# Performance work log

Hardware: AMD Instinct MI355X
Metric: run time of the kernel (lower is better)

Reference implementation:

```python
import jax, jax.numpy as jnp
import numpy as np

DEPTH = 8
INPUT_WIDTH = 64
INNER_WIDTH = 32
BATCH = 65536
N_NODES = 2 ** DEPTH - 1   # 255 inner nodes
N_LEAVES = 2 ** DEPTH      # 256 bins
EPS = 1e-8


def _tree_paths(depth):
    """For each leaf, the inner-node index at each level and whether the path
    goes right (right child uses 1 - decision, mirroring hstack([p, 1-p]) indexing)."""
    node_idx = np.zeros((2 ** depth, depth), dtype=np.int32)
    is_right = np.zeros((2 ** depth, depth), dtype=bool)
    for leaf in range(2 ** depth):
        idx = 0
        for level in range(depth):
            bit = (leaf >> (depth - 1 - level)) & 1
            node_idx[leaf, level] = idx
            is_right[leaf, level] = bool(bit)
            idx = 2 * idx + 1 + bit
    return node_idx, is_right

_NODE_IDX_NP, _IS_RIGHT_NP = _tree_paths(DEPTH)
NODE_IDX = jnp.asarray(_NODE_IDX_NP)   # [L, depth]
IS_RIGHT = jnp.asarray(_IS_RIGHT_NP)   # [L, depth]


def _init_b_i():
    """Replicates PartialRadialLayer.init_tree_weights: thresholds evenly dividing [0,1],
    stored as logits so sigmoid(b_i) recovers the threshold."""
    b = np.zeros(N_NODES, dtype=np.float64)
    b[0] = -0.5
    used = 1
    for i in range(1, DEPTH):
        n_nodes = 2 ** i
        div = float(2 ** (i + 1))
        for node in range(n_nodes):
            b[used + node] = -(2 * node + 1) / div
        used += n_nodes
    return np.log(-b / (1.0 + b)).astype(np.float32).reshape(1, -1)


def setup_inputs() -> dict:
    key = jax.random.key(0)
    kx, kr, kt = jax.random.split(key, 3)
    x = jax.random.normal(kx, (BATCH, INPUT_WIDTH), dtype=jnp.float32)
    # kaiming_normal_ on [1, input_width]: fan_in = input_width
    ray = jax.random.normal(kr, (1, INPUT_WIDTH), dtype=jnp.float32) * np.sqrt(2.0 / INPUT_WIDTH)
    # kaiming_normal_ on [L, I, W]: fan_in = I * W
    inner_transforms = jax.random.normal(kt, (N_LEAVES, INPUT_WIDTH, INNER_WIDTH), dtype=jnp.float32) * np.sqrt(2.0 / (INPUT_WIDTH * INNER_WIDTH))
    w_i = jnp.zeros((1, N_NODES), dtype=jnp.float32)
    a_i = 5.0 * jnp.ones((1, N_NODES), dtype=jnp.float32)
    b_i = jnp.asarray(_init_b_i())
    return {"x": x, "ray": ray, "inner_transforms": inner_transforms,
            "w_i": w_i, "b_i": b_i, "a_i": a_i}


def reference(x, ray, inner_transforms, w_i, b_i, a_i):
    # angles: arccos(cosine_similarity(x, ray)) / pi
    x_norm = jnp.maximum(jnp.linalg.norm(x, axis=1), EPS)            # [B]
    r_norm = jnp.maximum(jnp.linalg.norm(ray, axis=1), EPS)          # [1]
    cos = jnp.clip((x @ ray[0]) / (x_norm * r_norm), -1.0, 1.0)      # [B]
    angles = jnp.arccos(cos) / jnp.pi                                # [B]

    # per-node decisions
    node_fns = (0.5 + jax.nn.sigmoid(w_i)) * angles[:, None] - jax.nn.sigmoid(b_i)  # [B, N]
    decisions = jax.nn.sigmoid(node_fns * (1.0 + a_i))                               # [B, N]

    # soft bin distribution: product along each root-to-leaf path
    g = decisions[:, NODE_IDX]                       # [B, L, depth]
    vals = jnp.where(IS_RIGHT, 1.0 - g, g)           # right child -> 1 - p
    distribution = jnp.prod(vals, axis=2)            # [B, L]

    # weighted per-leaf transforms: einsum('bi,liw->blw') then ('bl,blo->bo'), fused
    out = jnp.einsum('bl,bi,liw->bw', distribution, x, inner_transforms)
    return out
```

## Files before the change

kernel.cpp:

```cpp
#include <hip/hip_runtime.h>
#include <hip/hip_bf16.h>

#define NLEAF 256
#define MBLK 256
#define THREADS 512

typedef __attribute__((ext_vector_type(4))) float f32x4;
typedef __attribute__((ext_vector_type(4))) unsigned int uint4v;
typedef __attribute__((ext_vector_type(8))) __bf16 bf16x8;
typedef __attribute__((ext_vector_type(4))) __bf16 bf16x4;

#define OFF_DIST 0
#define OFF_XP   131072
#define OFF_T    147456
#define OFF_AC   151552
#define OFF_BC   152576
#define OFF_ANG  153600
#define OFF_RAY  154624
#define SMEM_BYTES 154880

__device__ __forceinline__ float sigf(float s) { return 1.0f / (1.0f + __expf(-s)); }

__global__ void prep_T(const float* __restrict__ T, __bf16* __restrict__ wsT) {
  int gid = blockIdx.x * 256 + threadIdx.x;
  int l = gid >> 11;
  int rem = gid & 2047;
  int k = rem >> 5;
  int w = rem & 31;
  float v = T[gid];
  int off = (w * 128 + 2 * k) ^ ((w & 7) << 4);
  wsT[((size_t)l * 4096 + off) >> 1] = (__bf16)v;
}

template <bool USE_WS>
__global__ __launch_bounds__(THREADS, 2)
void prl_main(const float* __restrict__ x, const float* __restrict__ ray,
              const float* __restrict__ w_i, const float* __restrict__ b_i,
              const float* __restrict__ a_i, const void* __restrict__ tsrc,
              float* __restrict__ out) {
  extern __shared__ char smem[];
  const int tid = threadIdx.x;
  const int lane = tid & 63;
  const int wid = tid >> 6;
  const int g = lane >> 4;
  const int ln = lane & 15;
  const int row0 = blockIdx.x * MBLK;

  float* A_c = (float*)(smem + OFF_AC);
  float* B_c = (float*)(smem + OFF_BC);
  float* angles = (float*)(smem + OFF_ANG);
  float* ray_l = (float*)(smem + OFF_RAY);
  __bf16* distb = (__bf16*)(smem + OFF_DIST);

  if (tid < 255) {
    float aa = 1.0f + a_i[tid];
    A_c[tid] = (0.5f + sigf(w_i[tid])) * aa;
    B_c[tid] = -sigf(b_i[tid]) * aa;
  }
  if (tid >= 256 && tid < 320) ray_l[tid - 256] = ray[tid - 256];
  __syncthreads();

  bf16x8 afrag[2][2] = {};
  float* xp = (float*)(smem + OFF_XP);
  for (int c = 0; c < 4; ++c) {
    const float* xg = x + (size_t)(row0 + c * 64) * 64;
#pragma unroll
    for (int p = 0; p < 2; ++p) {
      int idx = p * 512 + tid;
      f32x4 v = *(const f32x4*)(xg + idx * 4);
      *(f32x4*)(xp + idx * 4) = v;
      int cg = idx & 15;
      f32x4 rv = *(const f32x4*)(ray_l + cg * 4);
      float a0 = v[0] * v[0] + v[1] * v[1] + v[2] * v[2] + v[3] * v[3];
      float a1 = v[0] * rv[0] + v[1] * rv[1] + v[2] * rv[2] + v[3] * rv[3];
      float a2 = rv[0] * rv[0] + rv[1] * rv[1] + rv[2] * rv[2] + rv[3] * rv[3];
#pragma unroll
      for (int s = 1; s < 16; s <<= 1) {
        a0 += __shfl_xor(a0, s, 64);
        a1 += __shfl_xor(a1, s, 64);
        a2 += __shfl_xor(a2, s, 64);
      }
      if ((tid & 15) == 0) {
        int r = idx >> 4;
        float xn = fmaxf(sqrtf(a0), 1e-8f);
        float rn = fmaxf(sqrtf(a2), 1e-8f);
        float cs = a1 / (xn * rn);
        cs = fminf(fmaxf(cs, -1.0f), 1.0f);
        angles[c * 64 + r] = acosf(cs) * 0.31830988618379067f;
      }
    }
    __syncthreads();
    if ((wid >> 1) == c) {
#pragma unroll
      for (int mt = 0; mt < 2; ++mt)
#pragma unroll
        for (int kt = 0; kt < 2; ++kt) {
          int rl = (wid & 1) * 32 + mt * 16 + ln;
          int k0 = kt * 32 + g * 8;
          f32x4 u0 = *(const f32x4*)(xp + rl * 64 + k0);
          f32x4 u1 = *(const f32x4*)(xp + rl * 64 + k0 + 4);
          bf16x8 af;
          af[0] = (__bf16)u0[0]; af[1] = (__bf16)u0[1];
          af[2] = (__bf16)u0[2]; af[3] = (__bf16)u0[3];
          af[4] = (__bf16)u1[0]; af[5] = (__bf16)u1[1];
          af[6] = (__bf16)u1[2]; af[7] = (__bf16)u1[3];
          afrag[mt][kt] = af;
        }
    }
    __syncthreads();
  }

  __bf16* PA = (__bf16*)(smem + OFF_XP);
  __bf16* PB = (__bf16*)(smem + OFF_XP + 8192);
  if (tid < 256) {
    float ang = angles[tid];
    float d = sigf(fmaf(A_c[0], ang, B_c[0]));
    PA[tid] = (__bf16)d;
    PA[256 + tid] = (__bf16)(1.0f - d);
  }
  __syncthreads();
  {
    int n = tid >> 8, r = tid & 255;
    float p = (float)PA[tid];
    float ang = angles[r];
    float d = sigf(fmaf(A_c[1 + n], ang, B_c[1 + n]));
    PB[(2 * n) * 256 + r] = (__bf16)(p * d);
    PB[(2 * n + 1) * 256 + r] = (__bf16)(p * (1.0f - d));
  }
  __syncthreads();
#pragma unroll
  for (int it = 0; it < 2; ++it) {
    int e = it * 512 + tid;
    int n = e >> 8, r = e & 255;
    float p = (float)PB[e];
    float ang = angles[r];
    float d = sigf(fmaf(A_c[3 + n], ang, B_c[3 + n]));
    PA[(2 * n) * 256 + r] = (__bf16)(p * d);
    PA[(2 * n + 1) * 256 + r] = (__bf16)(p * (1.0f - d));
  }
  __syncthreads();
#pragma unroll
  for (int it = 0; it < 4; ++it) {
    int e = it * 512 + tid;
    int n = e >> 8, r = e & 255;
    float p = (float)PA[e];
    float ang = angles[r];
    float d = sigf(fmaf(A_c[7 + n], ang, B_c[7 + n]));
    PB[(2 * n) * 256 + r] = (__bf16)(p * d);
    PB[(2 * n + 1) * 256 + r] = (__bf16)(p * (1.0f - d));
  }
  __syncthreads();
#pragma unroll
  for (int it = 0; it < 8; ++it) {
    int e = it * 512 + tid;
    int n4 = e >> 8, r = e & 255;
    float p4 = (float)PB[e];
    float ang = angles[r];
    float d4 = sigf(fmaf(A_c[15 + n4], ang, B_c[15 + n4]));
    float p5[2] = {p4 * d4, p4 * (1.0f - d4)};
#pragma unroll
    for (int b5 = 0; b5 < 2; ++b5) {
      int n5 = 2 * n4 + b5;
      float d5 = sigf(fmaf(A_c[31 + n5], ang, B_c[31 + n5]));
      float p6[2] = {p5[b5] * d5, p5[b5] * (1.0f - d5)};
#pragma unroll
      for (int b6 = 0; b6 < 2; ++b6) {
        int n6 = 2 * n5 + b6;
        float d6 = sigf(fmaf(A_c[63 + n6], ang, B_c[63 + n6]));
        float p7[2] = {p6[b6] * d6, p6[b6] * (1.0f - d6)};
#pragma unroll
        for (int b7 = 0; b7 < 2; ++b7) {
          int n7 = 2 * n6 + b7;
          float d7 = sigf(fmaf(A_c[127 + n7], ang, B_c[127 + n7]));
          float pv = p7[b7];
          distb[(2 * n7) * 256 + r] = (__bf16)(pv * d7);
          distb[(2 * n7 + 1) * 256 + r] = (__bf16)(pv * (1.0f - d7));
        }
      }
    }
  }

  f32x4 acc[2][2] = {};
  const int strip = wid * 32;
  char* tb = smem + OFF_T;

  uint4v tv = {};
  f32x4 tvf = {};
  if constexpr (USE_WS) {
    if (tid < 256) tv = *(const uint4v*)((const char*)tsrc + tid * 16);
  } else {
    tvf = *(const f32x4*)((const float*)tsrc + tid * 4);
  }

  for (int l = 0; l < NLEAF; ++l) {
    __syncthreads();
    if constexpr (USE_WS) {
      if (tid < 256) *(uint4v*)(tb + tid * 16) = tv;
    } else {
      int e4 = tid * 4, k = e4 >> 5, wb = e4 & 31;
#pragma unroll
      for (int j = 0; j < 4; ++j) {
        int w = wb + j;
        int ad = (w * 128 + 2 * k) ^ ((w & 7) << 4);
        *(__bf16*)(tb + ad) = (__bf16)tvf[j];
      }
    }
    __syncthreads();
    if (l + 1 < NLEAF) {
      if constexpr (USE_WS) {
        if (tid < 256)
          tv = *(const uint4v*)((const char*)tsrc + (size_t)(l + 1) * 4096 + tid * 16);
      } else {
        tvf = *(const f32x4*)((const float*)tsrc + (size_t)(l + 1) * 2048 + tid * 4);
      }
    }
    bf16x8 bf[2][2];
#pragma unroll
    for (int kt = 0; kt < 2; ++kt)
#pragma unroll
      for (int nt = 0; nt < 2; ++nt) {
        int w = nt * 16 + ln;
        int ad = (w * 128 + kt * 64 + g * 16) ^ ((w & 7) << 4);
        bf[kt][nt] = *(const bf16x8*)(tb + ad);
      }
    f32x4 dv[2];
#pragma unroll
    for (int mt = 0; mt < 2; ++mt) {
      int row = strip + mt * 16 + g * 4;
      bf16x4 dd = *(const bf16x4*)(distb + l * 256 + row);
      dv[mt] = (f32x4){(float)dd[0], (float)dd[1], (float)dd[2], (float)dd[3]};
    }
    f32x4 zero = {0.0f, 0.0f, 0.0f, 0.0f};
#pragma unroll
    for (int mt = 0; mt < 2; ++mt)
#pragma unroll
      for (int nt = 0; nt < 2; ++nt) {
        f32x4 y = __builtin_amdgcn_mfma_f32_16x16x32_bf16(afrag[mt][0], bf[0][nt], zero, 0, 0, 0);
        y = __builtin_amdgcn_mfma_f32_16x16x32_bf16(afrag[mt][1], bf[1][nt], y, 0, 0, 0);
        acc[mt][nt] += dv[mt] * y;
      }
  }

#pragma unroll
  for (int mt = 0; mt < 2; ++mt)
#pragma unroll
    for (int nt = 0; nt < 2; ++nt)
#pragma unroll
      for (int e = 0; e < 4; ++e) {
        int row = row0 + strip + mt * 16 + g * 4 + e;
        out[(size_t)row * 32 + nt * 16 + ln] = acc[mt][nt][e];
      }
}

extern "C" void kernel_launch(void* const* d_in, const int* in_sizes, int n_in,
                              void* d_out, int out_size, void* d_ws, size_t ws_size,
                              hipStream_t stream) {
  const float* x = (const float*)d_in[0];
  const float* ray = (const float*)d_in[1];
  const float* T = (const float*)d_in[2];
  const float* w_i = (const float*)d_in[3];
  const float* b_i = (const float*)d_in[4];
  const float* a_i = (const float*)d_in[5];
  float* out = (float*)d_out;

  bool use_ws = ws_size >= (size_t)NLEAF * 4096;
  if (use_ws) {
    hipFuncSetAttribute(reinterpret_cast<const void*>(&prl_main<true>),
                        hipFuncAttributeMaxDynamicSharedMemorySize, SMEM_BYTES);
    prep_T<<<2048, 256, 0, stream>>>(T, (__bf16*)d_ws);
    prl_main<true><<<256, THREADS, SMEM_BYTES, stream>>>(x, ray, w_i, b_i, a_i, d_ws, out);
  } else {
    hipFuncSetAttribute(reinterpret_cast<const void*>(&prl_main<false>),
                        hipFuncAttributeMaxDynamicSharedMemorySize, SMEM_BYTES);
    prl_main<false><<<256, THREADS, SMEM_BYTES, stream>>>(x, ray, w_i, b_i, a_i, T, out);
  }
}
```

Baseline: 180.1 us.

## Double-buffer leaf transform tiles in LDS and coalesce prep_T writes

The main loop now keeps two LDS buffers for the per-leaf bf16 transform tile. The next leaf's tile is written while the current one feeds the MFMAs, so each iteration needs one barrier instead of two. prep_T is rewritten to use one block per leaf: it stages the swizzled tile in shared memory and writes it out as coalesced 16-byte stores instead of scattered 2-byte stores. The cost is 4 KB more LDS per block, which could affect occupancy at two blocks per CU.

Result: faster. 163.8 us (-9.1%).

```diff
diff --git a/kernel.cpp b/kernel.cpp
--- a/kernel.cpp
+++ b/kernel.cpp
@@ -13,23 +13,34 @@
 #define OFF_DIST 0
 #define OFF_XP   131072
 #define OFF_T    147456
-#define OFF_AC   151552
-#define OFF_BC   152576
-#define OFF_ANG  153600
-#define OFF_RAY  154624
-#define SMEM_BYTES 154880
+#define OFF_AC   155648
+#define OFF_BC   156672
+#define OFF_ANG  157696
+#define OFF_RAY  158720
+#define SMEM_BYTES 158976
 
 __device__ __forceinline__ float sigf(float s) { return 1.0f / (1.0f + __expf(-s)); }
 
-__global__ void prep_T(const float* __restrict__ T, __bf16* __restrict__ wsT) {
-  int gid = blockIdx.x * 256 + threadIdx.x;
-  int l = gid >> 11;
-  int rem = gid & 2047;
-  int k = rem >> 5;
-  int w = rem & 31;
-  float v = T[gid];
-  int off = (w * 128 + 2 * k) ^ ((w & 7) << 4);
-  wsT[((size_t)l * 4096 + off) >> 1] = (__bf16)v;
+__global__ __launch_bounds__(256) void prep_T(const float* __restrict__ T,
+                                              __bf16* __restrict__ wsT) {
+  __shared__ char tile[4096];
+  const int l = blockIdx.x;
+  const float* src = T + (size_t)l * 2048;
+  const int t = threadIdx.x;
+#pragma unroll
+  for (int p = 0; p < 2; ++p) {
+    int e = p * 1024 + t * 4;
+    f32x4 v = *(const f32x4*)(src + e);
+    int k = e >> 5, w0 = e & 31;
+#pragma unroll
+    for (int j = 0; j < 4; ++j) {
+      int w = w0 + j;
+      int off = (w * 128 + 2 * k) ^ ((w & 7) << 4);
+      *(__bf16*)(tile + off) = (__bf16)v[j];
+    }
+  }
+  __syncthreads();
+  *(uint4v*)((char*)wsT + (size_t)l * 4096 + t * 16) = *(const uint4v*)(tile + t * 16);
 }
 
 template <bool USE_WS>
@@ -187,16 +198,14 @@
   uint4v tv = {};
   f32x4 tvf = {};
   if constexpr (USE_WS) {
-    if (tid < 256) tv = *(const uint4v*)((const char*)tsrc + tid * 16);
+    if (tid < 256) {
+      tv = *(const uint4v*)((const char*)tsrc + tid * 16);
+      *(uint4v*)(tb + tid * 16) = tv;
+      tv = *(const uint4v*)((const char*)tsrc + 4096 + tid * 16);
+    }
   } else {
     tvf = *(const f32x4*)((const float*)tsrc + tid * 4);
-  }
-
-  for (int l = 0; l < NLEAF; ++l) {
-    __syncthreads();
-    if constexpr (USE_WS) {
-      if (tid < 256) *(uint4v*)(tb + tid * 16) = tv;
-    } else {
+    {
       int e4 = tid * 4, k = e4 >> 5, wb = e4 & 31;
 #pragma unroll
       for (int j = 0; j < 4; ++j) {
@@ -205,24 +214,32 @@
         *(__bf16*)(tb + ad) = (__bf16)tvf[j];
       }
     }
-    __syncthreads();
-    if (l + 1 < NLEAF) {
-      if constexpr (USE_WS) {
-        if (tid < 256)
-          tv = *(const uint4v*)((const char*)tsrc + (size_t)(l + 1) * 4096 + tid * 16);
-      } else {
-        tvf = *(const f32x4*)((const float*)tsrc + (size_t)(l + 1) * 2048 + tid * 4);
-      }
-    }
-    bf16x8 bf[2][2];
-#pragma unroll
-    for (int kt = 0; kt < 2; ++kt)
-#pragma unroll
-      for (int nt = 0; nt < 2; ++nt) {
-        int w = nt * 16 + ln;
-        int ad = (w * 128 + kt * 64 + g * 16) ^ ((w & 7) << 4);
-        bf[kt][nt] = *(const bf16x8*)(tb + ad);
-      }
+    tvf = *(const f32x4*)((const float*)tsrc + 2048 + tid * 4);
+  }
+  __syncthreads();
+
+  for (int l = 0; l < NLEAF; ++l) {
+    char* cur = tb + (l & 1) * 4096;
+    char* nxt = tb + ((l + 1) & 1) * 4096;
+    if constexpr (USE_WS) {
+      if (tid < 256) {
+        if (l + 1 < NLEAF) *(uint4v*)(nxt + tid * 16) = tv;
+        if (l + 2 < NLEAF)
+          tv = *(const uint4v*)((const char*)tsrc + (size_t)(l + 2) * 4096 + tid * 16);
+      }
+    } else {
+      if (l + 1 < NLEAF) {
+        int e4 = tid * 4, k = e4 >> 5, wb = e4 & 31;
+#pragma unroll
+        for (int j = 0; j < 4; ++j) {
+          int w = wb + j;
+          int ad = (w * 128 + 2 * k) ^ ((w & 7) << 4);
+          *(__bf16*)(nxt + ad) = (__bf16)tvf[j];
+        }
+      }
+      if (l + 2 < NLEAF)
+        tvf = *(const f32x4*)((const float*)tsrc + (size_t)(l + 2) * 2048 + tid * 4);
+    }
     f32x4 dv[2];
 #pragma unroll
     for (int mt = 0; mt < 2; ++mt) {
@@ -230,15 +247,25 @@
       bf16x4 dd = *(const bf16x4*)(distb + l * 256 + row);
       dv[mt] = (f32x4){(float)dd[0], (float)dd[1], (float)dd[2], (float)dd[3]};
     }
+    bf16x8 bfr[2][2];
+#pragma unroll
+    for (int kt = 0; kt < 2; ++kt)
+#pragma unroll
+      for (int nt = 0; nt < 2; ++nt) {
+        int w = nt * 16 + ln;
+        int ad = (w * 128 + kt * 64 + g * 16) ^ ((w & 7) << 4);
+        bfr[kt][nt] = *(const bf16x8*)(cur + ad);
+      }
     f32x4 zero = {0.0f, 0.0f, 0.0f, 0.0f};
 #pragma unroll
     for (int mt = 0; mt < 2; ++mt)
 #pragma unroll
       for (int nt = 0; nt < 2; ++nt) {
-        f32x4 y = __builtin_amdgcn_mfma_f32_16x16x32_bf16(afrag[mt][0], bf[0][nt], zero, 0, 0, 0);
-        y = __builtin_amdgcn_mfma_f32_16x16x32_bf16(afrag[mt][1], bf[1][nt], y, 0, 0, 0);
+        f32x4 y = __builtin_amdgcn_mfma_f32_16x16x32_bf16(afrag[mt][0], bfr[0][nt], zero, 0, 0, 0);
+        y = __builtin_amdgcn_mfma_f32_16x16x32_bf16(afrag[mt][1], bfr[1][nt], y, 0, 0, 0);
         acc[mt][nt] += dv[mt] * y;
       }
+    __syncthreads();
   }
 
 #pragma unroll
@@ -267,7 +294,7 @@
   if (use_ws) {
     hipFuncSetAttribute(reinterpret_cast<const void*>(&prl_main<true>),
                         hipFuncAttributeMaxDynamicSharedMemorySize, SMEM_BYTES);
-    prep_T<<<2048, 256, 0, stream>>>(T, (__bf16*)d_ws);
+    prep_T<<<256, 256, 0, stream>>>(T, (__bf16*)d_ws);
     prl_main<true><<<256, THREADS, SMEM_BYTES, stream>>>(x, ray, w_i, b_i, a_i, d_ws, out);
   } else {
     hipFuncSetAttribute(reinterpret_cast<const void*>(&prl_main<false>),
```
